# Performance work log

Hardware: AMD Instinct MI355X
Metric: run time of the kernel (lower is better)

## Reference

```python
import jax, jax.numpy as jnp
import numpy as np

EPS = 1e-10
TOP_K = 2  # experts_per_token


def setup_inputs() -> dict:
    key = jax.random.key(0)
    k1, k2 = jax.random.split(key)
    dim, E = 2048, 64
    B, S = 4, 4096
    x = jax.random.normal(k1, (B * S, dim), dtype=jnp.float32)
    W = jax.random.normal(k2, (dim, E), dtype=jnp.float32) * (1.0 / np.sqrt(dim))
    b = jnp.zeros((E,), dtype=jnp.float32)
    return {"x": x, "W": W, "b": b, "batch_size": B, "seq_len": S}


def reference(x, W, b, batch_size, seq_len):
    E = W.shape[1]
    N = x.shape[0]  # batch_size * seq_len
    # gate + softmax + clamp
    scores = jax.nn.softmax(x @ W + b, axis=1)
    scores = jnp.clip(scores, EPS, 1.0 - EPS)
    # log-odds transform and rz loss over (seq, experts) per batch
    logits = jnp.log(scores / (1.0 - scores)).reshape(batch_size, seq_len, E)
    rz_loss = jnp.mean(jax.scipy.special.logsumexp(logits, axis=(1, 2)))
    # top-k experts per token
    top_scores, sel_idx = jax.lax.top_k(scores, TOP_K)  # (N, K) each
    flat_idx = sel_idx.reshape(-1)  # (N*K,)
    # histogram of assignments per expert (torch.histc with unit bins)
    num_tokens_per_expert = jax.ops.segment_sum(
        jnp.ones_like(flat_idx, dtype=jnp.float32), flat_idx, num_segments=E)
    # stable argsort groups slots by expert id, preserving token order
    perm = jnp.argsort(flat_idx, stable=True)  # (N*K,)
    top_scores_sorted = top_scores.reshape(-1)[perm]
    token_indices_experts_sorted = perm // TOP_K
    return (top_scores_sorted, token_indices_experts_sorted,
            num_tokens_per_expert, rz_loss)
```

## Files before the change

### kernel.cpp

```cpp
#include <hip/hip_runtime.h>
#include <math.h>

#define EPS_ 1e-10f
#define MARGIN 4e-3f

typedef __attribute__((ext_vector_type(8))) short sh8;
typedef __attribute__((ext_vector_type(4))) float fx4;

__device__ __forceinline__ bool betterf(float v, int i, float w, int j) {
    return (v > w) || (v == w && i < j);
}
__device__ __forceinline__ bool betterd(double v, int i, double w, int j) {
    return (v > w) || (v == w && i < j);
}
__device__ __forceinline__ unsigned short f2bf(float f) {
    unsigned u = __float_as_uint(f);
    u += 0x7fffu + ((u >> 16) & 1u);
    return (unsigned short)(u >> 16);
}
__device__ __forceinline__ float bf2f(unsigned short h) {
    return __uint_as_float(((unsigned)h) << 16);
}

struct U2x2 { uint2 lo, hi; };

__global__ __launch_bounds__(256)
void wconv(const float* __restrict__ W, unsigned short* __restrict__ wf)
{
    const int gid = blockIdx.x * 256 + threadIdx.x;
    const int e = gid & 63, k = gid >> 6;
    const int s = k >> 5, kk = k & 31, bq = kk >> 3, j = kk & 7;
    const int t = e >> 4, n = e & 15;
    const int l = n + 16 * bq;
    const float w = W[(size_t)k * 64 + e];
    const unsigned short hi = f2bf(w);
    const unsigned short lo = f2bf(w - bf2f(hi));
    const size_t base = ((size_t)s * 4 + t) * 2;
    wf[(base + 0) * 512 + l * 8 + j] = hi;
    wf[(base + 1) * 512 + l * 8 + j] = lo;
}

#define ROWPAD 68
__global__ __launch_bounds__(256)
void gemm_fused(const float* __restrict__ x, const unsigned short* __restrict__ wfg,
                const float* __restrict__ b, int dim, int N,
                float* __restrict__ ts, int* __restrict__ sel,
                float* __restrict__ rzrow,
                int* __restrict__ nflags, int* __restrict__ flaglist)
{
    __shared__ unsigned short xh[2][64][ROWPAD];
    __shared__ unsigned short xl[2][64][ROWPAD];
    __shared__ unsigned short wfl[2][4096];

    const int tid  = threadIdx.x;
    const int lane = tid & 63;
    const int wv   = tid >> 6;
    const int r0   = blockIdx.x * 64;
    const int nstep = dim / 32;

    const int srow = tid >> 2;
    const int sk   = (tid & 3) * 8;

    const float* xp = x + (size_t)(r0 + srow) * dim + sk;

    fx4 acc[4] = {};

    {
        const float4 xa = *(const float4*)(xp);
        const float4 xb = *(const float4*)(xp + 4);
        const int4* wsrc = (const int4*)(wfg);
        const int4 wa = wsrc[tid * 2], wb = wsrc[tid * 2 + 1];
        unsigned short h[8], l[8];
        const float v[8] = {xa.x, xa.y, xa.z, xa.w, xb.x, xb.y, xb.z, xb.w};
#pragma unroll
        for (int c = 0; c < 8; ++c) { h[c] = f2bf(v[c]); l[c] = f2bf(v[c] - bf2f(h[c])); }
        uint2 h0, h1, l0, l1;
        h0.x = h[0] | ((unsigned)h[1] << 16); h0.y = h[2] | ((unsigned)h[3] << 16);
        h1.x = h[4] | ((unsigned)h[5] << 16); h1.y = h[6] | ((unsigned)h[7] << 16);
        l0.x = l[0] | ((unsigned)l[1] << 16); l0.y = l[2] | ((unsigned)l[3] << 16);
        l1.x = l[4] | ((unsigned)l[5] << 16); l1.y = l[6] | ((unsigned)l[7] << 16);
        *(uint2*)&xh[0][srow][sk]     = h0;
        *(uint2*)&xh[0][srow][sk + 4] = h1;
        *(uint2*)&xl[0][srow][sk]     = l0;
        *(uint2*)&xl[0][srow][sk + 4] = l1;
        *(int4*)&wfl[0][tid * 16]     = wa;
        *(int4*)&wfl[0][tid * 16 + 8] = wb;
    }
    __syncthreads();

    const int m  = lane & 15;
    const int bq = lane >> 4;

    for (int w = 0; w < nstep; ++w) {
        const int cur = w & 1;

        float4 xa, xb; int4 wa, wb;
        if (w + 1 < nstep) {
            xa = *(const float4*)(xp + (size_t)(w + 1) * 32);
            xb = *(const float4*)(xp + (size_t)(w + 1) * 32 + 4);
            const int4* wsrc = (const int4*)(wfg + (size_t)(w + 1) * 4096);
            wa = wsrc[tid * 2]; wb = wsrc[tid * 2 + 1];
        }

        U2x2 au, bu;
        const unsigned short* ah = &xh[cur][wv * 16 + m][bq * 8];
        const unsigned short* al = &xl[cur][wv * 16 + m][bq * 8];
        au.lo = *(const uint2*)ah; au.hi = *(const uint2*)(ah + 4);
        bu.lo = *(const uint2*)al; bu.hi = *(const uint2*)(al + 4);
        const sh8 ahi = __builtin_bit_cast(sh8, au);
        const sh8 alo = __builtin_bit_cast(sh8, bu);
#pragma unroll
        for (int t = 0; t < 4; ++t) {
            const sh8 bhi = __builtin_bit_cast(sh8,
                *(const int4*)&wfl[cur][(t * 2 + 0) * 512 + lane * 8]);
            const sh8 blo = __builtin_bit_cast(sh8,
                *(const int4*)&wfl[cur][(t * 2 + 1) * 512 + lane * 8]);
            acc[t] = __builtin_amdgcn_mfma_f32_16x16x32_bf16(ahi, bhi, acc[t], 0, 0, 0);
            acc[t] = __builtin_amdgcn_mfma_f32_16x16x32_bf16(ahi, blo, acc[t], 0, 0, 0);
            acc[t] = __builtin_amdgcn_mfma_f32_16x16x32_bf16(alo, bhi, acc[t], 0, 0, 0);
        }

        if (w + 1 < nstep) {
            const int nb2 = cur ^ 1;
            unsigned short h[8], l[8];
            const float v[8] = {xa.x, xa.y, xa.z, xa.w, xb.x, xb.y, xb.z, xb.w};
#pragma unroll
            for (int c = 0; c < 8; ++c) { h[c] = f2bf(v[c]); l[c] = f2bf(v[c] - bf2f(h[c])); }
            uint2 h0, h1, l0, l1;
            h0.x = h[0] | ((unsigned)h[1] << 16); h0.y = h[2] | ((unsigned)h[3] << 16);
            h1.x = h[4] | ((unsigned)h[5] << 16); h1.y = h[6] | ((unsigned)h[7] << 16);
            l0.x = l[0] | ((unsigned)l[1] << 16); l0.y = l[2] | ((unsigned)l[3] << 16);
            l1.x = l[4] | ((unsigned)l[5] << 16); l1.y = l[6] | ((unsigned)l[7] << 16);
            *(uint2*)&xh[nb2][srow][sk]     = h0;
            *(uint2*)&xh[nb2][srow][sk + 4] = h1;
            *(uint2*)&xl[nb2][srow][sk]     = l0;
            *(uint2*)&xl[nb2][srow][sk + 4] = l1;
            *(int4*)&wfl[nb2][tid * 16]     = wa;
            *(int4*)&wfl[nb2][tid * 16 + 8] = wb;
        }
        __syncthreads();
    }

    const int n = lane & 15;
    const int g = lane >> 4;
    float bb[4];
#pragma unroll
    for (int t = 0; t < 4; ++t) bb[t] = b[t * 16 + n];

#pragma unroll
    for (int i = 0; i < 4; ++i) {
        const int row = r0 + wv * 16 + g * 4 + i;
        float z[4];
#pragma unroll
        for (int t = 0; t < 4; ++t) z[t] = acc[t][i] + bb[t];

        float v1 = -3.4e38f, v2 = -3.4e38f;
        int i1 = 1 << 30, i2 = 1 << 30;
#pragma unroll
        for (int t = 0; t < 4; ++t) {
            const float v = z[t];
            const int e = t * 16 + n;
            if (v > v1)      { v2 = v1; i2 = i1; v1 = v; i1 = e; }
            else if (v > v2) { v2 = v;  i2 = e; }
        }
#pragma unroll
        for (int mm = 1; mm < 16; mm <<= 1) {
            const float w1 = __shfl_xor(v1, mm, 16); const int j1 = __shfl_xor(i1, mm, 16);
            const float w2 = __shfl_xor(v2, mm, 16); const int j2 = __shfl_xor(i2, mm, 16);
            if (betterf(w1, j1, v1, i1)) {
                float nv2; int ni2;
                if (betterf(v1, i1, w2, j2)) { nv2 = v1; ni2 = i1; }
                else                         { nv2 = w2; ni2 = j2; }
                v1 = w1; i1 = j1; v2 = nv2; i2 = ni2;
            } else if (betterf(w1, j1, v2, i2)) { v2 = w1; i2 = j1; }
        }

        float m3 = -3.4e38f;
#pragma unroll
        for (int t = 0; t < 4; ++t) {
            const int e = t * 16 + n;
            const bool skip = (e == i1) || (e == i2);
            m3 = skip ? m3 : fmaxf(m3, z[t]);
        }
#pragma unroll
        for (int mm = 1; mm < 16; mm <<= 1) m3 = fmaxf(m3, __shfl_xor(m3, mm, 16));

        float sloc[4], ssum = 0.0f;
#pragma unroll
        for (int t = 0; t < 4; ++t) { sloc[t] = expf(z[t] - v1); ssum += sloc[t]; }
#pragma unroll
        for (int mm = 1; mm < 16; mm <<= 1) ssum += __shfl_xor(ssum, mm, 16);
        const float inv = 1.0f / ssum;
        float srz = 0.0f;
#pragma unroll
        for (int t = 0; t < 4; ++t) {
            float sc = fminf(fmaxf(sloc[t] * inv, EPS_), 1.0f - EPS_);
            srz += sc / (1.0f - sc);
        }
#pragma unroll
        for (int mm = 1; mm < 16; mm <<= 1) srz += __shfl_xor(srz, mm, 16);

        if (n == 0) {
            const float s1 = fminf(fmaxf(inv, EPS_), 1.0f - EPS_);
            const float s2 = fminf(fmaxf(expf(v2 - v1) * inv, EPS_), 1.0f - EPS_);
            ts[row * 2 + 0] = s1;
            ts[row * 2 + 1] = s2;
            sel[row * 2 + 0] = i1;
            sel[row * 2 + 1] = i2;
            rzrow[row] = srz;
            if ((v1 - v2) < MARGIN || (v2 - m3) < MARGIN) {
                const int slot = atomicAdd(nflags, 1);
                flaglist[slot] = row;
            }
        }
    }
}

__global__ __launch_bounds__(1024)
void fixup(const float* __restrict__ x, const float* __restrict__ W,
           const float* __restrict__ b, int dim,
           const int* __restrict__ nflags, const int* __restrict__ flaglist,
           float* __restrict__ ts, int* __restrict__ sel)
{
    __shared__ double red[1024];
    const int tid = threadIdx.x;
    const int e = tid & 63;
    const int q = tid >> 6;
    const int nf = *nflags;
    const int slice = dim >> 4;

    for (int f = blockIdx.x; f < nf; f += gridDim.x) {
        const int row = flaglist[f];
        const float* xr = x + (size_t)row * dim;
        const int k0 = q * slice;
        double a0 = 0.0, a1 = 0.0, a2 = 0.0, a3 = 0.0;
        for (int k = k0; k < k0 + slice; k += 4) {
            a0 = fma((double)xr[k + 0], (double)W[(size_t)(k + 0) * 64 + e], a0);
            a1 = fma((double)xr[k + 1], (double)W[(size_t)(k + 1) * 64 + e], a1);
            a2 = fma((double)xr[k + 2], (double)W[(size_t)(k + 2) * 64 + e], a2);
            a3 = fma((double)xr[k + 3], (double)W[(size_t)(k + 3) * 64 + e], a3);
        }
        red[tid] = (a0 + a1) + (a2 + a3);
        __syncthreads();
        for (int st = 512; st >= 64; st >>= 1) {
            if (tid < st) red[tid] += red[tid + st];
            __syncthreads();
        }
        if (tid < 64) {
            const double z = red[tid] + (double)b[e];
            double v1 = z, v2 = -1e300;
            int i1 = e, i2 = 1 << 30;
#pragma unroll
            for (int mm = 1; mm < 64; mm <<= 1) {
                const double w1 = __shfl_xor(v1, mm, 64); const int j1 = __shfl_xor(i1, mm, 64);
                const double w2 = __shfl_xor(v2, mm, 64); const int j2 = __shfl_xor(i2, mm, 64);
                if (betterd(w1, j1, v1, i1)) {
                    double nv2; int ni2;
                    if (betterd(v1, i1, w2, j2)) { nv2 = v1; ni2 = i1; }
                    else                         { nv2 = w2; ni2 = j2; }
                    v1 = w1; i1 = j1; v2 = nv2; i2 = ni2;
                } else if (betterd(w1, j1, v2, i2)) { v2 = w1; i2 = j1; }
            }
            float sl = expf((float)(z - v1));
            float ssum = sl;
#pragma unroll
            for (int mm = 1; mm < 64; mm <<= 1) ssum += __shfl_xor(ssum, mm, 64);
            const float inv = 1.0f / ssum;
            if (e == 0) {
                const float s1 = fminf(fmaxf(inv, EPS_), 1.0f - EPS_);
                const float s2 = fminf(fmaxf(expf((float)(v2 - v1)) * inv, EPS_), 1.0f - EPS_);
                ts[row * 2 + 0] = s1;
                ts[row * 2 + 1] = s2;
                sel[row * 2 + 0] = i1;
                sel[row * 2 + 1] = i2;
            }
        }
        __syncthreads();
    }
}

__global__ void hist_chunks(const int* __restrict__ sel, int nchunks,
                            int* __restrict__ hist, int* __restrict__ cnt2)
{
    __shared__ int cnt[64];
    const int lane = threadIdx.x;
    const int c = blockIdx.x;
    cnt[lane] = 0;
    __syncthreads();
    const int ex = sel[c * 64 + lane];
    atomicAdd(&cnt[ex], 1);
    __syncthreads();
    cnt2[(size_t)lane * nchunks + c] = cnt[lane];
    if (cnt[lane]) atomicAdd(&hist[lane], cnt[lane]);
}

__global__ void rz_batch(const float* __restrict__ rzrow,
                         const int* __restrict__ bs_p, const int* __restrict__ sl_p,
                         double* __restrict__ bsum)
{
    __shared__ double red[256];
    const int nb = bs_p[0];
    const int seq = sl_p[0];
    for (int bb = blockIdx.x; bb < nb; bb += gridDim.x) {
        double s = 0.0;
        for (int i = threadIdx.x; i < seq; i += 256)
            s += (double)rzrow[(size_t)bb * seq + i];
        red[threadIdx.x] = s;
        __syncthreads();
        for (int st = 128; st > 0; st >>= 1) {
            if (threadIdx.x < st) red[threadIdx.x] += red[threadIdx.x + st];
            __syncthreads();
        }
        if (threadIdx.x == 0) bsum[bb] = red[0];
        __syncthreads();
    }
}

__global__ void combine(const int* __restrict__ hist,
                        int* __restrict__ estart,
                        const double* __restrict__ bsum,
                        const int* __restrict__ bs_p,
                        float* __restrict__ out_cnt, float* __restrict__ out_rz)
{
    const int e = threadIdx.x;
    const int c0 = hist[e];
    int incl = c0;
#pragma unroll
    for (int mm = 1; mm < 64; mm <<= 1) {
        const int w = __shfl_up(incl, mm, 64);
        if (e >= mm) incl += w;
    }
    estart[e] = incl - c0;
    out_cnt[e] = (float)c0;
    if (e == 0) {
        const int nb = bs_p[0];
        double a = 0.0;
        for (int i = 0; i < nb; ++i) a += log(bsum[i]);
        out_rz[0] = (float)(a / nb);
    }
}

__global__ __launch_bounds__(1024)
void chunk_scan(const int* __restrict__ cnt2, const int* __restrict__ estart,
                int nchunks, int* __restrict__ cbase)
{
    __shared__ int sc[1024];
    const int e = blockIdx.x;
    const int t = threadIdx.x;
    const int v = (t < nchunks) ? cnt2[(size_t)e * nchunks + t] : 0;
    sc[t] = v;
    __syncthreads();
#pragma unroll
    for (int off = 1; off < 1024; off <<= 1) {
        const int add = (t >= off) ? sc[t - off] : 0;
        __syncthreads();
        sc[t] += add;
        __syncthreads();
    }
    if (t < nchunks)
        cbase[(size_t)t * 64 + e] = estart[e] + sc[t] - v;
}

__global__ void scatter(const int* __restrict__ sel, const float* __restrict__ ts,
                        const int* __restrict__ cbase,
                        float* __restrict__ out_sc, float* __restrict__ out_idx)
{
    __shared__ int shx[64];
    const int lane = threadIdx.x;
    const int c = blockIdx.x;
    const int idx = c * 64 + lane;
    const int ex = sel[idx];
    shx[lane] = ex;
    __syncthreads();
    int pre = 0;
#pragma unroll
    for (int j = 0; j < 64; ++j) pre += (int)((j < lane) && (shx[j] == ex));
    const int pos = cbase[c * 64 + ex] + pre;
    out_sc[pos]  = ts[idx];
    out_idx[pos] = (float)(idx >> 1);
}

extern "C" void kernel_launch(void* const* d_in, const int* in_sizes, int n_in,
                              void* d_out, int out_size, void* d_ws, size_t ws_size,
                              hipStream_t stream)
{
    const float* x = (const float*)d_in[0];
    const float* W = (const float*)d_in[1];
    const float* b = (const float*)d_in[2];
    const int* bs_p = (const int*)d_in[3];
    const int* sl_p = (const int*)d_in[4];

    const int E   = in_sizes[2];
    const int dim = in_sizes[1] / E;
    const int N   = in_sizes[0] / dim;
    const int total = N * 2;
    const int nchunks = total / 64;

    char* ws = (char*)d_ws;
    size_t off = 0;
    int*    hist     = (int*)(ws + off); off += 256;
    double* bsum     = (double*)(ws + off); off += 512;
    int*    nflags   = (int*)(ws + off); off += 256;
    int*    estart   = (int*)(ws + off); off += 256;
    float*  ts       = (float*)(ws + off); off += (size_t)total * 4;
    int*    sel      = (int*)(ws + off); off += (size_t)total * 4;
    int*    flaglist = (int*)(ws + off); off += (size_t)N * 4;
    float*  rzrow    = (float*)(ws + off); off += (size_t)N * 4;
    int*    cnt2     = (int*)(ws + off); off += (size_t)nchunks * 64 * 4;
    int*    cbase    = (int*)(ws + off); off += (size_t)nchunks * 64 * 4;
    unsigned short* wfg = (unsigned short*)(ws + off); off += (size_t)dim * 64 * 2 * 2;

    float* out_sc  = (float*)d_out;
    float* out_idx = out_sc + total;
    float* out_cnt = out_idx + total;
    float* out_rz  = out_cnt + E;

    hipMemsetAsync(ws, 0, 1280, stream);

    hipLaunchKernelGGL(wconv, dim3(dim * 64 / 256), dim3(256), 0, stream, W, wfg);
    hipLaunchKernelGGL(gemm_fused, dim3(N / 64), dim3(256), 0, stream,
                       x, wfg, b, dim, N, ts, sel, rzrow, nflags, flaglist);
    hipLaunchKernelGGL(fixup, dim3(512), dim3(1024), 0, stream,
                       x, W, b, dim, nflags, flaglist, ts, sel);
    hipLaunchKernelGGL(hist_chunks, dim3(nchunks), dim3(64), 0, stream,
                       sel, nchunks, hist, cnt2);
    hipLaunchKernelGGL(rz_batch, dim3(64), dim3(256), 0, stream,
                       rzrow, bs_p, sl_p, bsum);
    hipLaunchKernelGGL(combine, dim3(1), dim3(64), 0, stream,
                       hist, estart, bsum, bs_p, out_cnt, out_rz);
    hipLaunchKernelGGL(chunk_scan, dim3(64), dim3(1024), 0, stream,
                       cnt2, estart, nchunks, cbase);
    hipLaunchKernelGGL(scatter, dim3(nchunks), dim3(64), 0, stream,
                       sel, ts, cbase, out_sc, out_idx);
}
```

Baseline: 110.1 us.

## Split-K GEMM across waves with direct register loads, dropping LDS staging

The gate GEMM kernel now gives each block 16 rows and splits the K dimension across its four waves. Each wave loads x and the pre-swizzled bf16 weights straight from global memory into registers, and the partial accumulators are reduced through shared memory at the end. This removes the double-buffered LDS staging and the per-step block barriers, and quadruples the block count to raise parallelism. In exchange, each weight fragment is now read from global/L2 by every wave instead of once per 64-row block, so weight traffic grows and three of the four waves sit idle during the epilogue.

```diff
diff --git a/kernel.cpp b/kernel.cpp
--- a/kernel.cpp
+++ b/kernel.cpp
@@ -21,8 +21,15 @@
 __device__ __forceinline__ float bf2f(unsigned short h) {
     return __uint_as_float(((unsigned)h) << 16);
 }
-
-struct U2x2 { uint2 lo, hi; };
+__device__ __forceinline__ void cvt8(const float4 a, const float4 c, sh8& hi, sh8& lo) {
+    const float v[8] = {a.x, a.y, a.z, a.w, c.x, c.y, c.z, c.w};
+#pragma unroll
+    for (int j = 0; j < 8; ++j) {
+        const unsigned short h = f2bf(v[j]);
+        hi[j] = (short)h;
+        lo[j] = (short)f2bf(v[j] - bf2f(h));
+    }
+}
 
 __global__ __launch_bounds__(256)
 void wconv(const float* __restrict__ W, unsigned short* __restrict__ wf)
@@ -40,106 +47,79 @@
     wf[(base + 1) * 512 + l * 8 + j] = lo;
 }
 
-#define ROWPAD 68
-__global__ __launch_bounds__(256)
-void gemm_fused(const float* __restrict__ x, const unsigned short* __restrict__ wfg,
-                const float* __restrict__ b, int dim, int N,
-                float* __restrict__ ts, int* __restrict__ sel,
-                float* __restrict__ rzrow,
-                int* __restrict__ nflags, int* __restrict__ flaglist)
-{
-    __shared__ unsigned short xh[2][64][ROWPAD];
-    __shared__ unsigned short xl[2][64][ROWPAD];
-    __shared__ unsigned short wfl[2][4096];
+#define NKS 4
+__global__ __launch_bounds__(256, 4)
+void gemm_mfma(const float* __restrict__ x, const unsigned short* __restrict__ wfg,
+               const float* __restrict__ b, int dim, int N,
+               float* __restrict__ ts, int* __restrict__ sel,
+               float* __restrict__ rzrow,
+               int* __restrict__ nflags, int* __restrict__ flaglist)
+{
+    __shared__ float red[3][64][17];
 
     const int tid  = threadIdx.x;
     const int lane = tid & 63;
     const int wv   = tid >> 6;
-    const int r0   = blockIdx.x * 64;
-    const int nstep = dim / 32;
-
-    const int srow = tid >> 2;
-    const int sk   = (tid & 3) * 8;
-
-    const float* xp = x + (size_t)(r0 + srow) * dim + sk;
+    const int r0   = blockIdx.x * 16;
+    const int kslice = dim / NKS;
+    const int k0   = wv * kslice;
+    const int nstep = kslice / 32;
+
+    const int m = lane & 15;
+    const int q = lane >> 4;
 
     fx4 acc[4] = {};
 
-    {
-        const float4 xa = *(const float4*)(xp);
-        const float4 xb = *(const float4*)(xp + 4);
-        const int4* wsrc = (const int4*)(wfg);
-        const int4 wa = wsrc[tid * 2], wb = wsrc[tid * 2 + 1];
-        unsigned short h[8], l[8];
-        const float v[8] = {xa.x, xa.y, xa.z, xa.w, xb.x, xb.y, xb.z, xb.w};
-#pragma unroll
-        for (int c = 0; c < 8; ++c) { h[c] = f2bf(v[c]); l[c] = f2bf(v[c] - bf2f(h[c])); }
-        uint2 h0, h1, l0, l1;
-        h0.x = h[0] | ((unsigned)h[1] << 16); h0.y = h[2] | ((unsigned)h[3] << 16);
-        h1.x = h[4] | ((unsigned)h[5] << 16); h1.y = h[6] | ((unsigned)h[7] << 16);
-        l0.x = l[0] | ((unsigned)l[1] << 16); l0.y = l[2] | ((unsigned)l[3] << 16);
-        l1.x = l[4] | ((unsigned)l[5] << 16); l1.y = l[6] | ((unsigned)l[7] << 16);
-        *(uint2*)&xh[0][srow][sk]     = h0;
-        *(uint2*)&xh[0][srow][sk + 4] = h1;
-        *(uint2*)&xl[0][srow][sk]     = l0;
-        *(uint2*)&xl[0][srow][sk + 4] = l1;
-        *(int4*)&wfl[0][tid * 16]     = wa;
-        *(int4*)&wfl[0][tid * 16 + 8] = wb;
-    }
-    __syncthreads();
-
-    const int m  = lane & 15;
-    const int bq = lane >> 4;
+    const float* xp = x + (size_t)(r0 + m) * dim + k0 + q * 8;
+    const unsigned short* wbase = wfg + ((size_t)(k0 / 32) * 4096) + lane * 8;
+
+    float4 xa = *(const float4*)xp;
+    float4 xb = *(const float4*)(xp + 4);
 
     for (int w = 0; w < nstep; ++w) {
-        const int cur = w & 1;
-
-        float4 xa, xb; int4 wa, wb;
+        sh8 ahi, alo;
+        cvt8(xa, xb, ahi, alo);
+
         if (w + 1 < nstep) {
             xa = *(const float4*)(xp + (size_t)(w + 1) * 32);
             xb = *(const float4*)(xp + (size_t)(w + 1) * 32 + 4);
-            const int4* wsrc = (const int4*)(wfg + (size_t)(w + 1) * 4096);
-            wa = wsrc[tid * 2]; wb = wsrc[tid * 2 + 1];
-        }
-
-        U2x2 au, bu;
-        const unsigned short* ah = &xh[cur][wv * 16 + m][bq * 8];
-        const unsigned short* al = &xl[cur][wv * 16 + m][bq * 8];
-        au.lo = *(const uint2*)ah; au.hi = *(const uint2*)(ah + 4);
-        bu.lo = *(const uint2*)al; bu.hi = *(const uint2*)(al + 4);
-        const sh8 ahi = __builtin_bit_cast(sh8, au);
-        const sh8 alo = __builtin_bit_cast(sh8, bu);
+        }
+
+        const unsigned short* wk = wbase + (size_t)w * 4096;
+        sh8 bhi[4], blo[4];
 #pragma unroll
         for (int t = 0; t < 4; ++t) {
-            const sh8 bhi = __builtin_bit_cast(sh8,
-                *(const int4*)&wfl[cur][(t * 2 + 0) * 512 + lane * 8]);
-            const sh8 blo = __builtin_bit_cast(sh8,
-                *(const int4*)&wfl[cur][(t * 2 + 1) * 512 + lane * 8]);
-            acc[t] = __builtin_amdgcn_mfma_f32_16x16x32_bf16(ahi, bhi, acc[t], 0, 0, 0);
-            acc[t] = __builtin_amdgcn_mfma_f32_16x16x32_bf16(ahi, blo, acc[t], 0, 0, 0);
-            acc[t] = __builtin_amdgcn_mfma_f32_16x16x32_bf16(alo, bhi, acc[t], 0, 0, 0);
-        }
-
-        if (w + 1 < nstep) {
-            const int nb2 = cur ^ 1;
-            unsigned short h[8], l[8];
-            const float v[8] = {xa.x, xa.y, xa.z, xa.w, xb.x, xb.y, xb.z, xb.w};
-#pragma unroll
-            for (int c = 0; c < 8; ++c) { h[c] = f2bf(v[c]); l[c] = f2bf(v[c] - bf2f(h[c])); }
-            uint2 h0, h1, l0, l1;
-            h0.x = h[0] | ((unsigned)h[1] << 16); h0.y = h[2] | ((unsigned)h[3] << 16);
-            h1.x = h[4] | ((unsigned)h[5] << 16); h1.y = h[6] | ((unsigned)h[7] << 16);
-            l0.x = l[0] | ((unsigned)l[1] << 16); l0.y = l[2] | ((unsigned)l[3] << 16);
-            l1.x = l[4] | ((unsigned)l[5] << 16); l1.y = l[6] | ((unsigned)l[7] << 16);
-            *(uint2*)&xh[nb2][srow][sk]     = h0;
-            *(uint2*)&xh[nb2][srow][sk + 4] = h1;
-            *(uint2*)&xl[nb2][srow][sk]     = l0;
-            *(uint2*)&xl[nb2][srow][sk + 4] = l1;
-            *(int4*)&wfl[nb2][tid * 16]     = wa;
-            *(int4*)&wfl[nb2][tid * 16 + 8] = wb;
-        }
-        __syncthreads();
-    }
+            bhi[t] = __builtin_bit_cast(sh8, *(const int4*)(wk + (t * 2 + 0) * 512));
+            blo[t] = __builtin_bit_cast(sh8, *(const int4*)(wk + (t * 2 + 1) * 512));
+        }
+#pragma unroll
+        for (int t = 0; t < 4; ++t)
+            acc[t] = __builtin_amdgcn_mfma_f32_16x16x32_bf16(ahi, bhi[t], acc[t], 0, 0, 0);
+#pragma unroll
+        for (int t = 0; t < 4; ++t)
+            acc[t] = __builtin_amdgcn_mfma_f32_16x16x32_bf16(ahi, blo[t], acc[t], 0, 0, 0);
+#pragma unroll
+        for (int t = 0; t < 4; ++t)
+            acc[t] = __builtin_amdgcn_mfma_f32_16x16x32_bf16(alo, bhi[t], acc[t], 0, 0, 0);
+    }
+
+    if (wv > 0) {
+#pragma unroll
+        for (int t = 0; t < 4; ++t)
+#pragma unroll
+            for (int i = 0; i < 4; ++i)
+                red[wv - 1][lane][t * 4 + i] = acc[t][i];
+    }
+    __syncthreads();
+    if (wv != 0) return;
+
+#pragma unroll
+    for (int s = 0; s < 3; ++s)
+#pragma unroll
+        for (int t = 0; t < 4; ++t)
+#pragma unroll
+            for (int i = 0; i < 4; ++i)
+                acc[t][i] += red[s][lane][t * 4 + i];
 
     const int n = lane & 15;
     const int g = lane >> 4;
@@ -149,7 +129,7 @@
 
 #pragma unroll
     for (int i = 0; i < 4; ++i) {
-        const int row = r0 + wv * 16 + g * 4 + i;
+        const int row = r0 + g * 4 + i;
         float z[4];
 #pragma unroll
         for (int t = 0; t < 4; ++t) z[t] = acc[t][i] + bb[t];
@@ -418,7 +398,7 @@
     hipMemsetAsync(ws, 0, 1280, stream);
 
     hipLaunchKernelGGL(wconv, dim3(dim * 64 / 256), dim3(256), 0, stream, W, wfg);
-    hipLaunchKernelGGL(gemm_fused, dim3(N / 64), dim3(256), 0, stream,
+    hipLaunchKernelGGL(gemm_mfma, dim3(N / 16), dim3(256), 0, stream,
                        x, wfg, b, dim, N, ts, sel, rzrow, nflags, flaglist);
     hipLaunchKernelGGL(fixup, dim3(512), dim3(1024), 0, stream,
                        x, W, b, dim, nflags, flaglist, ts, sel);
```

Result: faster. 102.4 us (-7.0%).
